# Optimization experiments

Measured on AMD Instinct MI355X. Metric: run time of the kernel, lower is better.

## Reference

```python
import jax, jax.numpy as jnp
import numpy as np

EMBED_DIM = 1024
NUM_HEADS = 16
HEAD_DIM = EMBED_DIM // NUM_HEADS


def setup_inputs() -> dict:
    key = jax.random.key(0)
    ks = jax.random.split(key, 11)
    D = EMBED_DIM
    s = 1.0 / np.sqrt(D)
    x = jax.random.normal(ks[0], (2, 2048, D), dtype=jnp.float32)
    # nn.Linear weights are [out, in]; we store transposed [in, out] for x @ W.
    Wq = jax.random.uniform(ks[1], (D, D), jnp.float32, -s, s)
    bq = jax.random.uniform(ks[2], (D,), jnp.float32, -s, s)
    Wk = jax.random.uniform(ks[3], (D, D), jnp.float32, -s, s)
    bk = jax.random.uniform(ks[4], (D,), jnp.float32, -s, s)
    Wv = jax.random.uniform(ks[5], (D, D), jnp.float32, -s, s)
    bv = jax.random.uniform(ks[6], (D,), jnp.float32, -s, s)
    Wo = jax.random.uniform(ks[7], (D, D), jnp.float32, -s, s)
    bo = jax.random.uniform(ks[8], (D,), jnp.float32, -s, s)
    ln_g = jnp.ones((D,), jnp.float32)
    ln_b = jnp.zeros((D,), jnp.float32)
    return {"x": x, "Wq": Wq, "bq": bq, "Wk": Wk, "bk": bk,
            "Wv": Wv, "bv": bv, "Wo": Wo, "bo": bo,
            "ln_g": ln_g, "ln_b": ln_b}


def _layernorm(x, g, b, eps=1e-5):
    mu = jnp.mean(x, axis=-1, keepdims=True)
    var = jnp.mean(jnp.square(x - mu), axis=-1, keepdims=True)
    return (x - mu) * jax.lax.rsqrt(var + eps) * g + b


def reference(x, Wq, bq, Wk, bk, Wv, bv, Wo, bo, ln_g, ln_b):
    B, T, D = x.shape
    H, Hd = NUM_HEADS, HEAD_DIM
    # [B,T,D] -> [B,H,T,Hd]
    def split_heads(y):
        return y.reshape(B, T, H, Hd).transpose(0, 2, 1, 3)
    q = split_heads(x @ Wq + bq)
    k = split_heads(x @ Wk + bk)
    v = split_heads(x @ Wv + bv)
    scores = jnp.einsum('bhqd,bhkd->bhqk', q, k) / jnp.sqrt(jnp.float32(Hd))
    attn = jax.nn.softmax(scores, axis=-1)
    o = jnp.einsum('bhqk,bhkd->bhqd', attn, v)
    o = o.transpose(0, 2, 1, 3).reshape(B, T, D)
    out = o @ Wo + bo
    return _layernorm(out + x, ln_g, ln_b)
```

## Files before the change

kernel.cpp:

```cpp
#include <hip/hip_runtime.h>
#include <hip/hip_bf16.h>
#include <stdint.h>
#include <math.h>

#define B_ 2
#define T_ 2048
#define D_ 1024
#define H_ 16
#define HD_ 64
#define M_ 4096

using bf16 = __hip_bfloat16;
using short8 = __attribute__((ext_vector_type(8))) short;
using f32x4 = __attribute__((ext_vector_type(4))) float;

__device__ __forceinline__ void async16(const void* g, void* l) {
  __builtin_amdgcn_global_load_lds((const __attribute__((address_space(1))) void*)g,
                                   (__attribute__((address_space(3))) void*)l, 16, 0, 0);
}

__global__ __launch_bounds__(256) void prep_kernel(const float* __restrict__ wq, const float* __restrict__ wk,
                                                   const float* __restrict__ wv, const float* __restrict__ wo,
                                                   const float* __restrict__ x,
                                                   bf16* __restrict__ wt, bf16* __restrict__ xb) {
  const int z = blockIdx.z;
  const int tx = threadIdx.x, ty = threadIdx.y;
  if (z < 4) {
    __shared__ float tile[32][33];
    const float* src = z==0?wq:z==1?wk:z==2?wv:wo;
    bf16* dst = wt + ((size_t)z << 20);
    const int row0 = blockIdx.y*32;
    const int col  = blockIdx.x*32 + tx;
    #pragma unroll
    for (int j=ty; j<32; j+=8) tile[j][tx] = src[(size_t)(row0+j)*D_ + col];
    __syncthreads();
    const int ocol  = row0 + tx;
    const int orow0 = blockIdx.x*32;
    #pragma unroll
    for (int j=ty; j<32; j+=8) dst[(size_t)(orow0+j)*D_ + ocol] = __float2bfloat16(tile[tx][j]);
  } else {
    const int tid = ty*32 + tx;
    const size_t base = ((size_t)(blockIdx.y*32 + blockIdx.x))*4096 + (size_t)tid*16;
    #pragma unroll
    for (int h=0; h<2; ++h) {
      float4 a = *(const float4*)(x + base + h*8);
      float4 b = *(const float4*)(x + base + h*8 + 4);
      bf16 o[8] = { __float2bfloat16(a.x), __float2bfloat16(a.y), __float2bfloat16(a.z), __float2bfloat16(a.w),
                    __float2bfloat16(b.x), __float2bfloat16(b.y), __float2bfloat16(b.z), __float2bfloat16(b.w) };
      *(uint4*)(xb + base + h*8) = *(const uint4*)o;
    }
  }
}

__global__ __launch_bounds__(256,1) void qkv_gemm(const bf16* __restrict__ X, const bf16* __restrict__ Wt,
                                                  const float* __restrict__ bq, const float* __restrict__ bk,
                                                  const float* __restrict__ bv,
                                                  bf16* __restrict__ Qb, bf16* __restrict__ Kb, bf16* __restrict__ Vb) {
  __shared__ bf16 As[128*64];
  __shared__ bf16 Bs[128*64];
  const int tid = threadIdx.x;
  const int lane = tid & 63, wave = tid >> 6;
  const int quad = lane >> 4, l16 = lane & 15;
  const int wm = (wave >> 1) * 64, wn = (wave & 1) * 64;
  const int m0  = blockIdx.x * 128;
  const int nt0 = blockIdx.y * 128;
  const int which = nt0 >> 10;
  const int n0 = nt0 & 1023;
  const bf16* W = Wt + ((size_t)which << 20);
  const float* bias = which==0 ? bq : (which==1 ? bk : bv);
  const bool vmode = (which == 2);
  const float oscale = (which==0) ? 0.125f * 1.44269504088896340736f : 1.0f;

  f32x4 acc[4][4];
  #pragma unroll
  for (int i=0;i<4;i++)
    #pragma unroll
    for (int j=0;j<4;j++) acc[i][j] = (f32x4){0.f,0.f,0.f,0.f};

  for (int k0 = 0; k0 < 1024; k0 += 64) {
    __syncthreads();
    #pragma unroll
    for (int it=0; it<4; ++it) {
      int id = tid + it*256;
      int row = id >> 3, seg = id & 7;
      int c = ((seg ^ (row & 7)) << 3);
      async16(X + (size_t)(m0+row)*1024 + k0 + c, (char*)As + id*16);
      async16(W + (size_t)(n0+row)*1024 + k0 + c, (char*)Bs + id*16);
    }
    __syncthreads();
    const bf16* Asrc = vmode ? Bs : As;
    const bf16* Bsrc = vmode ? As : Bs;
    #pragma unroll
    for (int ks=0; ks<2; ++ks) {
      short8 af[4], bfv[4];
      #pragma unroll
      for (int i=0;i<4;i++) {
        const int row = wm + i*16 + l16;
        af[i] = *(const short8*)(Asrc + row*64 + (((ks*4+quad) ^ (row&7)) << 3));
      }
      #pragma unroll
      for (int j=0;j<4;j++) {
        const int row = wn + j*16 + l16;
        bfv[j] = *(const short8*)(Bsrc + row*64 + (((ks*4+quad) ^ (row&7)) << 3));
      }
      #pragma unroll
      for (int i=0;i<4;i++)
        #pragma unroll
        for (int j=0;j<4;j++)
          acc[i][j] = __builtin_amdgcn_mfma_f32_16x16x32_bf16(af[i], bfv[j], acc[i][j], 0, 0, 0);
    }
  }

  if (!vmode) {
    bf16* out = (which==0) ? Qb : Kb;
    #pragma unroll
    for (int i=0;i<4;i++) {
      #pragma unroll
      for (int j=0;j<4;j++) {
        const int n = n0 + wn + j*16 + l16;
        const float bvv = bias[n];
        const int h = n >> 6, hd = n & 63;
        #pragma unroll
        for (int r=0;r<4;r++) {
          const int m = m0 + wm + i*16 + quad*4 + r;
          const int b = m >> 11, t = m & 2047;
          out[(((size_t)b*H_ + h)*T_ + t)*HD_ + hd] = __float2bfloat16((acc[i][j][r] + bvv) * oscale);
        }
      }
    }
  } else {
    #pragma unroll
    for (int i=0;i<4;i++) {
      #pragma unroll
      for (int r=0;r<4;r++) {
        const int n = n0 + wm + i*16 + quad*4 + r;
        const float bvv = bias[n];
        const int h = n >> 6, hd = n & 63;
        #pragma unroll
        for (int j=0;j<4;j++) {
          const int m = m0 + wn + j*16 + l16;
          const int b = m >> 11, t = m & 2047;
          Vb[(((size_t)b*H_ + h)*HD_ + hd)*T_ + t] = __float2bfloat16(acc[i][j][r] + bvv);
        }
      }
    }
  }
}

__device__ __forceinline__ void stage64x64(const bf16* __restrict__ g, size_t gstride, bf16* lds,
                                           int wave, int lane) {
  const int lr = lane >> 3;
  const int c  = (lane & 7) ^ lr;
  #pragma unroll
  for (int it = 0; it < 2; ++it) {
    const int group = wave * 2 + it;
    async16(g + (size_t)(group*8 + lr)*gstride + c*8, lds + group*512 + lane*8);
  }
}

__device__ __forceinline__ short8 read_swz(const bf16* lds, int row, int chunk) {
  return *(const short8*)(lds + row*64 + ((chunk ^ (row & 7)) << 3));
}

#define PSTR 36

__global__ __launch_bounds__(256,2) void attn_kernel(const bf16* __restrict__ Qg, const bf16* __restrict__ Kg,
                                                     const bf16* __restrict__ Vg, bf16* __restrict__ Og) {
  __shared__ bf16 Qs[128*64];
  __shared__ bf16 Kd[2][64*64];
  __shared__ bf16 Vd[2][64*64];
  __shared__ bf16 Ps[4][4][16*PSTR];
  __shared__ float Lred[2][2][4][16];

  const int tid = threadIdx.x;
  const int lane = tid & 63, wave = tid >> 6;
  const int quad = lane >> 4, l16 = lane & 15;
  const int qhalf = wave & 1, khalf = wave >> 1;
  const int bh = blockIdx.y;
  const int q0 = blockIdx.x * 128;

  const bf16* Qp = Qg + (size_t)bh*T_*HD_;
  const bf16* Kp = Kg + (size_t)bh*T_*HD_;
  const bf16* Vp = Vg + (size_t)bh*HD_*T_;

  stage64x64(Qp + (size_t)q0*HD_,      HD_, Qs,       wave, lane);
  stage64x64(Qp + (size_t)(q0+64)*HD_, HD_, Qs+64*64, wave, lane);
  stage64x64(Kp, HD_, Kd[0], wave, lane);
  stage64x64(Vp, T_,  Vd[0], wave, lane);
  __syncthreads();

  short8 qf[4][2];
  #pragma unroll
  for (int s=0; s<4; ++s)
    #pragma unroll
    for (int ks=0; ks<2; ++ks)
      qf[s][ks] = read_swz(Qs, qhalf*64 + s*16 + l16, ks*4 + quad);

  f32x4 o_acc[4][4];
  float l_part[4] = {0.f, 0.f, 0.f, 0.f};
  #pragma unroll
  for (int s=0;s<4;s++)
    #pragma unroll
    for (int jv=0;jv<4;jv++) o_acc[s][jv] = (f32x4){0.f,0.f,0.f,0.f};

  const int krow = khalf * 32;
  const int NT = T_/64;

  for (int kt=0; kt<NT; ++kt) {
    const int cur = kt & 1;
    if (kt+1 < NT) {
      stage64x64(Kp + (size_t)(kt+1)*64*HD_, HD_, Kd[1-cur], wave, lane);
      stage64x64(Vp + (size_t)(kt+1)*64,     T_,  Vd[1-cur], wave, lane);
    }
    const bf16* Ks  = Kd[cur];
    const bf16* Vts = Vd[cur];

    short8 kf[2][2];
    #pragma unroll
    for (int jb=0; jb<2; ++jb)
      #pragma unroll
      for (int ks=0; ks<2; ++ks)
        kf[jb][ks] = read_swz(Ks, krow + jb*16 + l16, ks*4 + quad);
    short8 vf[4];
    #pragma unroll
    for (int jv=0; jv<4; ++jv)
      vf[jv] = read_swz(Vts, jv*16 + l16, khalf*4 + quad);

    #pragma unroll
    for (int s=0; s<4; ++s) {
      f32x4 sc[2];
      sc[0] = (f32x4){0.f,0.f,0.f,0.f};
      sc[1] = (f32x4){0.f,0.f,0.f,0.f};
      #pragma unroll
      for (int ks=0; ks<2; ++ks)
        #pragma unroll
        for (int jb=0; jb<2; ++jb)
          sc[jb] = __builtin_amdgcn_mfma_f32_16x16x32_bf16(kf[jb][ks], qf[s][ks], sc[jb], 0, 0, 0);
      bf16* Pw = &Ps[wave][s][0];
      #pragma unroll
      for (int jb=0; jb<2; ++jb) {
        bf16 pk[4];
        #pragma unroll
        for (int r=0; r<4; ++r) {
          float pv = __builtin_amdgcn_exp2f(sc[jb][r]);
          l_part[s] += pv;
          pk[r] = __float2bfloat16(pv);
        }
        *(uint2*)(&Pw[l16*PSTR + jb*16 + quad*4]) = *(const uint2*)pk;
      }
    }

    #pragma unroll
    for (int s=0; s<4; ++s) {
      short8 pf = *(const short8*)(&Ps[wave][s][l16*PSTR + quad*8]);
      #pragma unroll
      for (int jv=0; jv<4; ++jv)
        o_acc[s][jv] = __builtin_amdgcn_mfma_f32_16x16x32_bf16(pf, vf[jv], o_acc[s][jv], 0, 0, 0);
    }

    __syncthreads();
  }

  #pragma unroll
  for (int s=0; s<4; ++s) {
    float l = l_part[s];
    l += __shfl_xor(l, 16);
    l += __shfl_xor(l, 32);
    l_part[s] = l;
  }
  if (lane < 16) {
    #pragma unroll
    for (int s=0; s<4; ++s) Lred[qhalf][khalf][s][lane] = l_part[s];
  }
  __syncthreads();
  float linv[4][4];
  #pragma unroll
  for (int s=0; s<4; ++s)
    #pragma unroll
    for (int r=0; r<4; ++r)
      linv[s][r] = 1.0f / (Lred[qhalf][0][s][quad*4+r] + Lred[qhalf][1][s][quad*4+r]);

  f32x4* xb = (f32x4*)Qs;
  #pragma unroll
  for (int round=0; round<2; ++round) {
    const int sB = round*2;
    if (khalf == 1) {
      #pragma unroll
      for (int s2=0; s2<2; ++s2)
        #pragma unroll
        for (int jv=0; jv<4; ++jv)
          xb[qhalf*512 + s2*256 + jv*64 + lane] = o_acc[sB+s2][jv];
    }
    __syncthreads();
    if (khalf == 0) {
      #pragma unroll
      for (int s2=0; s2<2; ++s2)
        #pragma unroll
        for (int jv=0; jv<4; ++jv)
          o_acc[sB+s2][jv] += xb[qhalf*512 + s2*256 + jv*64 + lane];
    }
    __syncthreads();
  }

  if (khalf == 0) {
    const int b = bh >> 4, h = bh & 15;
    #pragma unroll
    for (int s=0; s<4; ++s)
      #pragma unroll
      for (int jv=0; jv<4; ++jv)
        #pragma unroll
        for (int r=0; r<4; ++r) {
          const int row = q0 + qhalf*64 + s*16 + quad*4 + r;
          const float ov = o_acc[s][jv][r] * linv[s][r];
          Og[((size_t)b*T_ + row)*D_ + h*HD_ + jv*16 + l16] = __float2bfloat16(ov);
        }
  }
}

__global__ __launch_bounds__(256,2) void proj_gemm(const bf16* __restrict__ A, const bf16* __restrict__ Wt,
                                                   const float* __restrict__ bo, const float* __restrict__ Xres,
                                                   float* __restrict__ tmp) {
  __shared__ bf16 As[128*64];
  __shared__ bf16 Bs[64*64];
  const int tid = threadIdx.x;
  const int lane = tid & 63, wave = tid >> 6;
  const int quad = lane >> 4, l16 = lane & 15;
  const int wm = wave * 32;
  const int m0 = blockIdx.x * 128;
  const int n0 = blockIdx.y * 64;

  f32x4 acc[2][4];
  #pragma unroll
  for (int i=0;i<2;i++)
    #pragma unroll
    for (int j=0;j<4;j++) acc[i][j] = (f32x4){0.f,0.f,0.f,0.f};

  for (int k0 = 0; k0 < 1024; k0 += 64) {
    __syncthreads();
    #pragma unroll
    for (int it=0; it<4; ++it) {
      int id = tid + it*256;
      int row = id >> 3, seg = id & 7;
      int c = ((seg ^ (row & 7)) << 3);
      async16(A + (size_t)(m0+row)*1024 + k0 + c, (char*)As + id*16);
    }
    #pragma unroll
    for (int it=0; it<2; ++it) {
      int id = tid + it*256;
      int row = id >> 3, seg = id & 7;
      int c = ((seg ^ (row & 7)) << 3);
      async16(Wt + (size_t)(n0+row)*1024 + k0 + c, (char*)Bs + id*16);
    }
    __syncthreads();
    #pragma unroll
    for (int ks=0; ks<2; ++ks) {
      short8 af[2], bfv[4];
      #pragma unroll
      for (int i=0;i<2;i++) {
        const int row = wm + i*16 + l16;
        af[i] = *(const short8*)(As + row*64 + (((ks*4+quad) ^ (row&7)) << 3));
      }
      #pragma unroll
      for (int j=0;j<4;j++) {
        const int row = j*16 + l16;
        bfv[j] = *(const short8*)(Bs + row*64 + (((ks*4+quad) ^ (row&7)) << 3));
      }
      #pragma unroll
      for (int i=0;i<2;i++)
        #pragma unroll
        for (int j=0;j<4;j++)
          acc[i][j] = __builtin_amdgcn_mfma_f32_16x16x32_bf16(af[i], bfv[j], acc[i][j], 0, 0, 0);
    }
  }

  #pragma unroll
  for (int i=0;i<2;i++) {
    #pragma unroll
    for (int j=0;j<4;j++) {
      const int n = n0 + j*16 + l16;
      const float bvv = bo[n];
      #pragma unroll
      for (int r=0;r<4;r++) {
        const int m = m0 + wm + i*16 + quad*4 + r;
        tmp[(size_t)m*1024 + n] = acc[i][j][r] + bvv + Xres[(size_t)m*1024 + n];
      }
    }
  }
}

__global__ __launch_bounds__(256) void ln_kernel(const float* __restrict__ tmp, const float* __restrict__ g,
                                                 const float* __restrict__ b, float* __restrict__ out) {
  const int row = blockIdx.x;
  const int tid = threadIdx.x;
  const float* p = tmp + (size_t)row*D_;
  float4 v = *(const float4*)(p + tid*4);
  float s  = v.x + v.y + v.z + v.w;
  float sq = v.x*v.x + v.y*v.y + v.z*v.z + v.w*v.w;
  #pragma unroll
  for (int off=32; off>0; off>>=1) { s += __shfl_down(s, off); sq += __shfl_down(sq, off); }
  __shared__ float red[8];
  __shared__ float stats[2];
  const int wave = tid >> 6, lane = tid & 63;
  if (lane == 0) { red[wave] = s; red[4+wave] = sq; }
  __syncthreads();
  if (tid == 0) {
    float S = red[0]+red[1]+red[2]+red[3];
    float Q = red[4]+red[5]+red[6]+red[7];
    float mu = S * (1.0f/D_);
    float var = Q * (1.0f/D_) - mu*mu;
    stats[0] = mu;
    stats[1] = rsqrtf(var + 1e-5f);
  }
  __syncthreads();
  const float mu = stats[0], rstd = stats[1];
  const float vals[4] = {v.x, v.y, v.z, v.w};
  float4 o;
  float* op = (float*)&o;
  #pragma unroll
  for (int c=0;c<4;c++) op[c] = (vals[c]-mu)*rstd*g[tid*4+c] + b[tid*4+c];
  *(float4*)(out + (size_t)row*D_ + tid*4) = o;
}

extern "C" void kernel_launch(void* const* d_in, const int* in_sizes, int n_in,
                              void* d_out, int out_size, void* d_ws, size_t ws_size,
                              hipStream_t stream) {
  (void)in_sizes; (void)n_in; (void)out_size; (void)ws_size;
  const float* x  = (const float*)d_in[0];
  const float* Wq = (const float*)d_in[1];
  const float* bq = (const float*)d_in[2];
  const float* Wk = (const float*)d_in[3];
  const float* bk = (const float*)d_in[4];
  const float* Wv = (const float*)d_in[5];
  const float* bv = (const float*)d_in[6];
  const float* Wo = (const float*)d_in[7];
  const float* bo = (const float*)d_in[8];
  const float* lg = (const float*)d_in[9];
  const float* lb = (const float*)d_in[10];
  float* out = (float*)d_out;

  char* ws = (char*)d_ws;
  bf16* wt  = (bf16*)ws;  ws += (size_t)4*1024*1024*sizeof(bf16);
  bf16* Xb  = (bf16*)ws;  ws += (size_t)M_*D_*sizeof(bf16);
  bf16* Vb  = (bf16*)ws;  ws += (size_t)M_*D_*sizeof(bf16);
  bf16* Ob  = (bf16*)ws;  ws += (size_t)M_*D_*sizeof(bf16);
  bf16* Qb  = (bf16*)ws;  ws += (size_t)M_*D_*sizeof(bf16);
  bf16* Kb  = (bf16*)ws;  ws += (size_t)M_*D_*sizeof(bf16);
  float* tmp = (float*)Qb;

  prep_kernel<<<dim3(32,32,5), dim3(32,8), 0, stream>>>(Wq, Wk, Wv, Wo, x, wt, Xb);
  qkv_gemm<<<dim3(32,24), 256, 0, stream>>>(Xb, wt, bq, bk, bv, Qb, Kb, Vb);
  attn_kernel<<<dim3(T_/128, B_*H_), 256, 0, stream>>>(Qb, Kb, Vb, Ob);
  proj_gemm<<<dim3(32,16), 256, 0, stream>>>(Ob, wt + (size_t)3*1024*1024, bo, x, tmp);
  ln_kernel<<<M_, 256, 0, stream>>>(tmp, lg, lb, out);
}
```

Baseline: 208.0 us.

## Feed softmax probabilities straight from registers into PV MFMA with K=16 instructions

```diff
diff --git a/kernel.cpp b/kernel.cpp
--- a/kernel.cpp
+++ b/kernel.cpp
@@ -12,11 +12,21 @@
 
 using bf16 = __hip_bfloat16;
 using short8 = __attribute__((ext_vector_type(8))) short;
+using s4 = __attribute__((ext_vector_type(4))) short;
 using f32x4 = __attribute__((ext_vector_type(4))) float;
 
 __device__ __forceinline__ void async16(const void* g, void* l) {
   __builtin_amdgcn_global_load_lds((const __attribute__((address_space(1))) void*)g,
                                    (__attribute__((address_space(3))) void*)l, 16, 0, 0);
+}
+
+__device__ __forceinline__ f32x4 mfma16(s4 a, s4 b, f32x4 c) {
+#if __has_builtin(__builtin_amdgcn_mfma_f32_16x16x16bf16_1k)
+  return __builtin_amdgcn_mfma_f32_16x16x16bf16_1k(a, b, c, 0, 0, 0);
+#else
+  asm("v_mfma_f32_16x16x16_bf16 %0, %1, %2, %0" : "+v"(c) : "v"(a), "v"(b));
+  return c;
+#endif
 }
 
 __global__ __launch_bounds__(256) void prep_kernel(const float* __restrict__ wq, const float* __restrict__ wk,
@@ -162,14 +172,18 @@
   return *(const short8*)(lds + row*64 + ((chunk ^ (row & 7)) << 3));
 }
 
-#define PSTR 36
+__device__ __forceinline__ s4 read_swz_b64(const bf16* lds, int row, int elem) {
+  const int chunk = elem >> 3;
+  const int sub   = elem & 7;
+  return *(const s4*)(lds + row*64 + ((chunk ^ (row & 7)) << 3) + sub);
+}
 
 __global__ __launch_bounds__(256,2) void attn_kernel(const bf16* __restrict__ Qg, const bf16* __restrict__ Kg,
                                                      const bf16* __restrict__ Vg, bf16* __restrict__ Og) {
   __shared__ bf16 Qs[128*64];
   __shared__ bf16 Kd[2][64*64];
   __shared__ bf16 Vd[2][64*64];
-  __shared__ bf16 Ps[4][4][16*PSTR];
+  __shared__ f32x4 Xch[1024];
   __shared__ float Lred[2][2][4][16];
 
   const int tid = threadIdx.x;
@@ -221,10 +235,12 @@
       #pragma unroll
       for (int ks=0; ks<2; ++ks)
         kf[jb][ks] = read_swz(Ks, krow + jb*16 + l16, ks*4 + quad);
-    short8 vf[4];
-    #pragma unroll
-    for (int jv=0; jv<4; ++jv)
-      vf[jv] = read_swz(Vts, jv*16 + l16, khalf*4 + quad);
+    s4 vf[2][4];
+    #pragma unroll
+    for (int jb=0; jb<2; ++jb)
+      #pragma unroll
+      for (int jv=0; jv<4; ++jv)
+        vf[jb][jv] = read_swz_b64(Vts, jv*16 + l16, krow + jb*16 + quad*4);
 
     #pragma unroll
     for (int s=0; s<4; ++s) {
@@ -236,7 +252,6 @@
         #pragma unroll
         for (int jb=0; jb<2; ++jb)
           sc[jb] = __builtin_amdgcn_mfma_f32_16x16x32_bf16(kf[jb][ks], qf[s][ks], sc[jb], 0, 0, 0);
-      bf16* Pw = &Ps[wave][s][0];
       #pragma unroll
       for (int jb=0; jb<2; ++jb) {
         bf16 pk[4];
@@ -246,16 +261,11 @@
           l_part[s] += pv;
           pk[r] = __float2bfloat16(pv);
         }
-        *(uint2*)(&Pw[l16*PSTR + jb*16 + quad*4]) = *(const uint2*)pk;
-      }
-    }
-
-    #pragma unroll
-    for (int s=0; s<4; ++s) {
-      short8 pf = *(const short8*)(&Ps[wave][s][l16*PSTR + quad*8]);
-      #pragma unroll
-      for (int jv=0; jv<4; ++jv)
-        o_acc[s][jv] = __builtin_amdgcn_mfma_f32_16x16x32_bf16(pf, vf[jv], o_acc[s][jv], 0, 0, 0);
+        const s4 pf = *(const s4*)pk;
+        #pragma unroll
+        for (int jv=0; jv<4; ++jv)
+          o_acc[s][jv] = mfma16(pf, vf[jb][jv], o_acc[s][jv]);
+      }
     }
 
     __syncthreads();
@@ -280,7 +290,6 @@
     for (int r=0; r<4; ++r)
       linv[s][r] = 1.0f / (Lred[qhalf][0][s][quad*4+r] + Lred[qhalf][1][s][quad*4+r]);
 
-  f32x4* xb = (f32x4*)Qs;
   #pragma unroll
   for (int round=0; round<2; ++round) {
     const int sB = round*2;
@@ -289,7 +298,7 @@
       for (int s2=0; s2<2; ++s2)
         #pragma unroll
         for (int jv=0; jv<4; ++jv)
-          xb[qhalf*512 + s2*256 + jv*64 + lane] = o_acc[sB+s2][jv];
+          Xch[qhalf*512 + s2*256 + jv*64 + lane] = o_acc[sB+s2][jv];
     }
     __syncthreads();
     if (khalf == 0) {
@@ -297,7 +306,7 @@
       for (int s2=0; s2<2; ++s2)
         #pragma unroll
         for (int jv=0; jv<4; ++jv)
-          o_acc[sB+s2][jv] += xb[qhalf*512 + s2*256 + jv*64 + lane];
+          o_acc[sB+s2][jv] += Xch[qhalf*512 + s2*256 + jv*64 + lane];
     }
     __syncthreads();
   }
```

After: 213.8 us. 1.03x slower.
